# Kernel tuning notes

Measured on AMD Instinct MI355X. Metric: run time of the kernel, lower is better.

## Reference

```python
import jax, jax.numpy as jnp
import numpy as np


def _cheb_conv(x, row, col, norm, W, b, num_nodes):
    # PyG ChebConv with sym normalization and lambda_max=2:
    # L_hat = -D^{-1/2} A D^{-1/2} (off-diagonal), diagonal exactly 0.
    # Tx_0 = x; Tx_1 = L_hat x; Tx_k = 2 L_hat Tx_{k-1} - Tx_{k-2}
    K = W.shape[0]
    Tx0 = x
    out = Tx0 @ W[0]
    Tx1 = jax.ops.segment_sum(norm[:, None] * Tx0[col], row, num_segments=num_nodes)
    out = out + Tx1 @ W[1]
    for k in range(2, K):
        Tx2 = 2.0 * jax.ops.segment_sum(norm[:, None] * Tx1[col], row, num_segments=num_nodes) - Tx0
        out = out + Tx2 @ W[k]
        Tx0, Tx1 = Tx1, Tx2
    return out + b


def setup_inputs() -> dict:
    key = jax.random.key(0)
    ks = jax.random.split(key, 8)
    N, E, D, H, C, K = 100000, 1600000, 128, 64, 5, 3
    x = jax.random.normal(ks[0], (N, D), dtype=jnp.float32)
    edge_index = jax.random.randint(ks[1], (2, E), 0, N, dtype=jnp.int64)
    edge_weight = jax.random.uniform(ks[2], (E,), dtype=jnp.float32)
    s1 = 1.0 / np.sqrt(D)
    s3 = 1.0 / np.sqrt(H)
    W1 = jax.random.normal(ks[3], (K, D, H), dtype=jnp.float32) * s1
    W3 = jax.random.normal(ks[4], (K, H, H), dtype=jnp.float32) * s3
    W4 = jax.random.normal(ks[5], (K, H, C), dtype=jnp.float32) * s3
    return {
        "x": x, "edge_index": edge_index, "edge_weight": edge_weight,
        "W1": W1, "b1": jnp.zeros((H,), jnp.float32),
        "W3": W3, "b3": jnp.zeros((H,), jnp.float32),
        "W4": W4, "b4": jnp.zeros((C,), jnp.float32),
    }


def reference(x, edge_index, edge_weight, W1, b1, W3, b3, W4, b4):
    N = x.shape[0]
    row, col = edge_index[0], edge_index[1]
    # symmetric normalization of the scaled Laplacian (lambda_max = 2)
    deg = jax.ops.segment_sum(edge_weight, row, num_segments=N)
    dinv = jnp.where(deg > 0, jax.lax.rsqrt(jnp.where(deg > 0, deg, 1.0)), 0.0)
    norm = -dinv[row] * edge_weight * dinv[col]
    # dropout is a no-op in eval mode (training=False)
    h = jax.nn.relu(_cheb_conv(x, row, col, norm, W1, b1, N))
    h = jax.nn.relu(_cheb_conv(h, row, col, norm, W3, b3, N))
    h = _cheb_conv(h, row, col, norm, W4, b4, N)
    return jax.nn.log_softmax(h, axis=1)
```

## Files before the change

### kernel.cpp

```cpp
#include <hip/hip_runtime.h>
#include <cstdint>
#include <cstddef>

typedef unsigned short u16;
typedef __attribute__((ext_vector_type(8))) short bf16x8;
typedef __attribute__((ext_vector_type(4))) float f32x4;

#define PB 1024
#define MAXSB 128

__device__ __forceinline__ float bflo(unsigned u) { return __uint_as_float(u << 16); }
__device__ __forceinline__ float bfhi(unsigned u) { return __uint_as_float(u & 0xFFFF0000u); }
__device__ __forceinline__ u16 f2bf(float f) {
    unsigned u = __float_as_uint(f);
    u += 0x7FFFu + ((u >> 16) & 1u);
    return (u16)(u >> 16);
}
__device__ __forceinline__ unsigned pack2(float a, float b) {
    return (unsigned)f2bf(a) | ((unsigned)f2bf(b) << 16);
}


__global__ __launch_bounds__(256) void binA(const int* __restrict__ row, int* __restrict__ P,
                                            int E, int NB, int EB) {
    __shared__ int hist[MAXSB];
    int b = blockIdx.x;
    if (threadIdx.x < MAXSB) hist[threadIdx.x] = 0;
    __syncthreads();
    int e0 = b * EB, e1 = min(E, e0 + EB);
    for (int e = e0 + threadIdx.x; e < e1; e += 256)
        atomicAdd(&hist[row[e] >> 10], 1);
    __syncthreads();
    if (threadIdx.x < NB) P[(size_t)threadIdx.x * PB + b] = hist[threadIdx.x];
}

__global__ __launch_bounds__(256) void binB1(int* __restrict__ P, int* __restrict__ bintot) {
    __shared__ int sh[256];
    int* p = P + (size_t)blockIdx.x * PB;
    int tid = threadIdx.x;
    int base = tid * 4;
    int v[4];
#pragma unroll
    for (int j = 0; j < 4; ++j) v[j] = p[base + j];
    int s = v[0] + v[1] + v[2] + v[3];
    sh[tid] = s;
    __syncthreads();
    for (int off = 1; off < 256; off <<= 1) {
        int t = (tid >= off) ? sh[tid - off] : 0;
        __syncthreads();
        sh[tid] += t;
        __syncthreads();
    }
    int run = sh[tid] - s;
#pragma unroll
    for (int j = 0; j < 4; ++j) { p[base + j] = run; run += v[j]; }
    if (tid == 255) bintot[blockIdx.x] = sh[255];
}

__global__ __launch_bounds__(256) void binC(const int* __restrict__ row, const int* __restrict__ col,
                                            const float* __restrict__ w, const int* __restrict__ P,
                                            const int* __restrict__ bintot, int2* __restrict__ rec,
                                            int E, int NB, int EB) {
    __shared__ int bs[MAXSB];
    __shared__ int cur[MAXSB];
    int b = blockIdx.x;
    int tid = threadIdx.x;
    if (tid < MAXSB) bs[tid] = (tid < NB) ? bintot[tid] : 0;
    __syncthreads();
    for (int off = 1; off < MAXSB; off <<= 1) {
        int t = (tid >= off && tid < MAXSB) ? bs[tid - off] : 0;
        __syncthreads();
        if (tid < MAXSB) bs[tid] += t;
        __syncthreads();
    }
    if (tid < NB) cur[tid] = (tid ? bs[tid - 1] : 0) + P[(size_t)tid * PB + b];
    __syncthreads();
    int e0 = b * EB, e1 = min(E, e0 + EB);
    for (int e = e0 + tid; e < e1; e += 256) {
        int r = row[e];
        int bin = r >> 10;
        int slot = atomicAdd(&cur[bin], 1);
        rec[slot] = make_int2(col[e] | ((r & 1023) << 17), __float_as_int(w[e]));
    }
}

__global__ __launch_bounds__(1024) void binD(const int2* __restrict__ rec,
                                             const int* __restrict__ bintot,
                                             int2* __restrict__ meta, int* __restrict__ rowp,
                                             float* __restrict__ dinv, int N, int NB) {
    __shared__ int bs[MAXSB];
    __shared__ int cnt[1024], st[1024], cur[1024];
    __shared__ float deg[1024];
    int bin = blockIdx.x;
    int tid = threadIdx.x;
    if (tid < MAXSB) bs[tid] = (tid < NB) ? bintot[tid] : 0;
    cnt[tid] = 0;
    deg[tid] = 0.f;
    __syncthreads();
    for (int off = 1; off < MAXSB; off <<= 1) {
        int t = (tid >= off && tid < MAXSB) ? bs[tid - off] : 0;
        __syncthreads();
        if (tid < MAXSB) bs[tid] += t;
        __syncthreads();
    }
    int e0 = bin ? bs[bin - 1] : 0;
    int e1 = bs[bin];
    __syncthreads();
    for (int e = e0 + tid; e < e1; e += 1024) {
        int2 v = rec[e];
        int rl = (v.x >> 17) & 1023;
        atomicAdd(&cnt[rl], 1);
        atomicAdd(&deg[rl], __int_as_float(v.y));
    }
    __syncthreads();
    st[tid] = cnt[tid];
    __syncthreads();
    for (int off = 1; off < 1024; off <<= 1) {
        int t = (tid >= off) ? st[tid - off] : 0;
        __syncthreads();
        st[tid] += t;
        __syncthreads();
    }
    int rows = min(1024, N - bin * 1024);
    int excl = st[tid] - cnt[tid];
    cur[tid] = e0 + excl;
    if (tid < rows) {
        rowp[bin * 1024 + tid] = e0 + excl;
        float d = deg[tid];
        dinv[bin * 1024 + tid] = d > 0.f ? rsqrtf(d) : 0.f;
    }
    if (bin == NB - 1 && tid == 0) rowp[N] = e1;
    __syncthreads();
    for (int e = e0 + tid; e < e1; e += 1024) {
        int2 v = rec[e];
        int rl = (v.x >> 17) & 1023;
        int slot = atomicAdd(&cur[rl], 1);
        meta[slot] = make_int2(v.x & 0x1FFFF, v.y);
    }
}

__global__ void scale_ev(const int* __restrict__ rowp, int2* __restrict__ meta,
                         const float* __restrict__ dinv, int n) {
    int r = blockIdx.x * blockDim.x + threadIdx.x;
    if (r >= n) return;
    int e0 = rowp[r], e1 = rowp[r + 1];
    float dr = dinv[r];
    int e = e0;
    for (; e + 4 <= e1; e += 4) {
        int2 v0 = meta[e], v1 = meta[e + 1], v2 = meta[e + 2], v3 = meta[e + 3];
        float d0 = dinv[v0.x], d1 = dinv[v1.x], d2 = dinv[v2.x], d3 = dinv[v3.x];
        v0.y = __float_as_int(-dr * __int_as_float(v0.y) * d0);
        v1.y = __float_as_int(-dr * __int_as_float(v1.y) * d1);
        v2.y = __float_as_int(-dr * __int_as_float(v2.y) * d2);
        v3.y = __float_as_int(-dr * __int_as_float(v3.y) * d3);
        meta[e] = v0; meta[e + 1] = v1; meta[e + 2] = v2; meta[e + 3] = v3;
    }
    for (; e < e1; ++e) {
        int2 v = meta[e];
        v.y = __float_as_int(-dr * __int_as_float(v.y) * dinv[v.x]);
        meta[e] = v;
    }
}

__global__ void prep(const float* __restrict__ x, unsigned* __restrict__ xb, int n2,
                     const float* __restrict__ W1, const float* __restrict__ W3,
                     const float* __restrict__ W4, u16* __restrict__ Wpu,
                     u16* __restrict__ Wp3, u16* __restrict__ Wpp) {
    int gi = blockIdx.x * blockDim.x + threadIdx.x;
    if (gi < 3072) {
        int idx = gi;
        int lane = idx & 63;
        int nt = (idx >> 6) % 12;
        int kt = idx / 768;
        int krow = kt * 32 + (lane >> 4) * 8;
        int c = nt * 16 + (lane & 15);
        u16 tmp[8];
#pragma unroll
        for (int j = 0; j < 8; ++j) {
            int k = krow + j;
            float v;
            if (c < 64)       v = W1[(size_t)k * 64 + c] - W1[2 * 8192 + (size_t)k * 64 + c];
            else if (c < 128) v = W1[8192 + (size_t)k * 64 + (c - 64)];
            else              v = W1[2 * 8192 + (size_t)k * 64 + (c - 128)];
            tmp[j] = f2bf(v);
        }
        *reinterpret_cast<uint4*>(Wpu + (size_t)idx * 8) = *reinterpret_cast<const uint4*>(tmp);
    } else if (gi < 3072 + 1536) {
        int idx = gi - 3072;
        int lane = idx & 63;
        int nt = (idx >> 6) & 3;
        int kt = idx >> 8;
        int krow = kt * 32 + (lane >> 4) * 8;
        int c = nt * 16 + (lane & 15);
        u16 tmp[8];
#pragma unroll
        for (int j = 0; j < 8; ++j) tmp[j] = f2bf(W3[(size_t)(krow + j) * 64 + c]);
        *reinterpret_cast<uint4*>(Wp3 + (size_t)idx * 8) = *reinterpret_cast<const uint4*>(tmp);
    } else if (gi < 3072 + 1536 + 256) {
        int idx = gi - (3072 + 1536);
        int lane = idx & 63;
        int nt = (idx >> 6) & 1;
        int kt = idx >> 7;
        int krow = kt * 32 + (lane >> 4) * 8;
        int c = nt * 16 + (lane & 15);
        u16 tmp[8];
#pragma unroll
        for (int j = 0; j < 8; ++j) {
            int k = krow + j;
            float v = 0.f;
            if (c < 5)                  v = W4[(size_t)k * 5 + c] - W4[640 + (size_t)k * 5 + c];
            else if (c >= 8 && c < 13)  v = W4[320 + (size_t)k * 5 + (c - 8)];
            else if (c >= 16 && c < 21) v = W4[640 + (size_t)k * 5 + (c - 16)];
            tmp[j] = f2bf(v);
        }
        *reinterpret_cast<uint4*>(Wpp + (size_t)idx * 8) = *reinterpret_cast<const uint4*>(tmp);
    } else {
        int i = gi - 4864;
        if (i < n2) {
            float2 v = reinterpret_cast<const float2*>(x)[i];
            xb[i] = pack2(v.x, v.y);
        }
    }
}

template <int MODE>
__global__ __launch_bounds__(256) void spmm64(const int* __restrict__ rp,
                                              const int2* __restrict__ meta,
                                              const u16* __restrict__ x,
                                              const u16* __restrict__ z,
                                              const float* __restrict__ bias,
                                              u16* __restrict__ y, int n) {
    int r = blockIdx.x * 32 + (threadIdx.x >> 3);
    if (r >= n) return;
    int f = (threadIdx.x & 7) * 8;
    int e0 = rp[r], e1 = rp[r + 1];
    float acc[8] = {0.f, 0.f, 0.f, 0.f, 0.f, 0.f, 0.f, 0.f};
    auto fma8 = [&](uint4 xv, float w) {
        acc[0] += w * bflo(xv.x); acc[1] += w * bfhi(xv.x);
        acc[2] += w * bflo(xv.y); acc[3] += w * bfhi(xv.y);
        acc[4] += w * bflo(xv.z); acc[5] += w * bfhi(xv.z);
        acc[6] += w * bflo(xv.w); acc[7] += w * bfhi(xv.w);
    };
    int e = e0;
    for (; e + 4 <= e1; e += 4) {
        int2 m0 = meta[e], m1 = meta[e + 1], m2 = meta[e + 2], m3 = meta[e + 3];
        uint4 v0 = *reinterpret_cast<const uint4*>(x + (size_t)m0.x * 64 + f);
        uint4 v1 = *reinterpret_cast<const uint4*>(x + (size_t)m1.x * 64 + f);
        uint4 v2 = *reinterpret_cast<const uint4*>(x + (size_t)m2.x * 64 + f);
        uint4 v3 = *reinterpret_cast<const uint4*>(x + (size_t)m3.x * 64 + f);
        fma8(v0, __int_as_float(m0.y));
        fma8(v1, __int_as_float(m1.y));
        fma8(v2, __int_as_float(m2.y));
        fma8(v3, __int_as_float(m3.y));
    }
    for (; e < e1; ++e) {
        int2 m = meta[e];
        uint4 xv = *reinterpret_cast<const uint4*>(x + (size_t)m.x * 64 + f);
        fma8(xv, __int_as_float(m.y));
    }
    if (MODE == 1 || MODE == 2) {
        uint4 zv = *reinterpret_cast<const uint4*>(z + (size_t)r * 64 + f);
        float zz[8] = {bflo(zv.x), bfhi(zv.x), bflo(zv.y), bfhi(zv.y),
                       bflo(zv.z), bfhi(zv.z), bflo(zv.w), bfhi(zv.w)};
#pragma unroll
        for (int j = 0; j < 8; ++j)
            acc[j] = (MODE == 1) ? 2.f * acc[j] + zz[j] : 2.f * acc[j] - zz[j];
    } else if (MODE == 3) {
        uint4 zv = *reinterpret_cast<const uint4*>(z + (size_t)r * 64 + f);
        float zz[8] = {bflo(zv.x), bfhi(zv.x), bflo(zv.y), bfhi(zv.y),
                       bflo(zv.z), bfhi(zv.z), bflo(zv.w), bfhi(zv.w)};
        float4 bl = *reinterpret_cast<const float4*>(bias + f);
        float4 bh = *reinterpret_cast<const float4*>(bias + f + 4);
        float bb[8] = {bl.x, bl.y, bl.z, bl.w, bh.x, bh.y, bh.z, bh.w};
#pragma unroll
        for (int j = 0; j < 8; ++j) acc[j] = fmaxf(acc[j] + zz[j] + bb[j], 0.f);
    }
    uint4 o;
    o.x = pack2(acc[0], acc[1]);
    o.y = pack2(acc[2], acc[3]);
    o.z = pack2(acc[4], acc[5]);
    o.w = pack2(acc[6], acc[7]);
    *reinterpret_cast<uint4*>(y + (size_t)r * 64 + f) = o;
}

__device__ __forceinline__ void spmm8_acc(const int* rp, const int2* meta, const u16* x,
                                          int r, int t, float* acc) {
    int e0 = rp[r], e1 = rp[r + 1];
    auto fma8 = [&](uint4 xv, float w) {
        acc[0] += w * bflo(xv.x); acc[1] += w * bfhi(xv.x);
        acc[2] += w * bflo(xv.y); acc[3] += w * bfhi(xv.y);
        acc[4] += w * bflo(xv.z); acc[5] += w * bfhi(xv.z);
        acc[6] += w * bflo(xv.w); acc[7] += w * bfhi(xv.w);
    };
    int e = e0 + t;
    for (; e + 4 < e1; e += 8) {
        int2 m0 = meta[e], m1 = meta[e + 4];
        uint4 v0 = *reinterpret_cast<const uint4*>(x + (size_t)m0.x * 8);
        uint4 v1 = *reinterpret_cast<const uint4*>(x + (size_t)m1.x * 8);
        fma8(v0, __int_as_float(m0.y));
        fma8(v1, __int_as_float(m1.y));
    }
    for (; e < e1; e += 4) {
        int2 m = meta[e];
        uint4 xv = *reinterpret_cast<const uint4*>(x + (size_t)m.x * 8);
        fma8(xv, __int_as_float(m.y));
    }
#pragma unroll
    for (int j = 0; j < 8; ++j) acc[j] += __shfl_xor(acc[j], 1);
#pragma unroll
    for (int j = 0; j < 8; ++j) acc[j] += __shfl_xor(acc[j], 2);
}

__global__ __launch_bounds__(256) void spmm8_p2(const int* __restrict__ rp,
                                                const int2* __restrict__ meta,
                                                const u16* __restrict__ x,
                                                const u16* __restrict__ z,
                                                u16* __restrict__ y, int n) {
    int r = blockIdx.x * 64 + (threadIdx.x >> 2);
    if (r >= n) return;
    int t = threadIdx.x & 3;
    float acc[8] = {0.f, 0.f, 0.f, 0.f, 0.f, 0.f, 0.f, 0.f};
    spmm8_acc(rp, meta, x, r, t, acc);
    if (t == 0) {
        uint4 zv = *reinterpret_cast<const uint4*>(z + (size_t)r * 8);
        float zz[8] = {bflo(zv.x), bfhi(zv.x), bflo(zv.y), bfhi(zv.y),
                       bflo(zv.z), bfhi(zv.z), bflo(zv.w), bfhi(zv.w)};
        uint4 o;
        o.x = pack2(2.f * acc[0] + zz[0], 2.f * acc[1] + zz[1]);
        o.y = pack2(2.f * acc[2] + zz[2], 2.f * acc[3] + zz[3]);
        o.z = pack2(2.f * acc[4] + zz[4], 2.f * acc[5] + zz[5]);
        o.w = pack2(2.f * acc[6] + zz[6], 2.f * acc[7] + zz[7]);
        *reinterpret_cast<uint4*>(y + (size_t)r * 8) = o;
    }
}

__global__ __launch_bounds__(256) void spmm8_lsm(const int* __restrict__ rp,
                                                 const int2* __restrict__ meta,
                                                 const u16* __restrict__ x,
                                                 const u16* __restrict__ z,
                                                 const float* __restrict__ bias,
                                                 float* __restrict__ out, int n) {
    int r = blockIdx.x * 64 + (threadIdx.x >> 2);
    if (r >= n) return;
    int t = threadIdx.x & 3;
    float acc[8] = {0.f, 0.f, 0.f, 0.f, 0.f, 0.f, 0.f, 0.f};
    spmm8_acc(rp, meta, x, r, t, acc);
    if (t == 0) {
        uint4 zv = *reinterpret_cast<const uint4*>(z + (size_t)r * 8);
        float zz[8] = {bflo(zv.x), bfhi(zv.x), bflo(zv.y), bfhi(zv.y),
                       bflo(zv.z), bfhi(zv.z), bflo(zv.w), bfhi(zv.w)};
        float val[5];
#pragma unroll
        for (int j = 0; j < 5; ++j) val[j] = acc[j] + zz[j] + bias[j];
        float mx = val[0];
#pragma unroll
        for (int j = 1; j < 5; ++j) mx = fmaxf(mx, val[j]);
        float s = 0.f;
#pragma unroll
        for (int j = 0; j < 5; ++j) s += expf(val[j] - mx);
        float l = logf(s);
#pragma unroll
        for (int j = 0; j < 5; ++j) out[(size_t)r * 5 + j] = val[j] - mx - l;
    }
}


__global__ __launch_bounds__(256) void gemm_u(const u16* __restrict__ A,
                                              const u16* __restrict__ Wp,
                                              u16* __restrict__ u0, u16* __restrict__ u1,
                                              u16* __restrict__ u2, int n) {
    int wave = threadIdx.x >> 6;
    int lane = threadIdx.x & 63;
    int r0 = blockIdx.x * 64 + wave * 16;
    int row = r0 + (lane & 15);
    int rowc = row < n ? row : n - 1;
    int kofs = (lane >> 4) * 8;
    f32x4 acc[12] = {};
    for (int kt = 0; kt < 4; ++kt) {
        bf16x8 a = *reinterpret_cast<const bf16x8*>(A + (size_t)rowc * 128 + kt * 32 + kofs);
        const u16* wb = Wp + (size_t)kt * 12 * 512 + (size_t)lane * 8;
#pragma unroll
        for (int nt = 0; nt < 12; ++nt) {
            bf16x8 b = *reinterpret_cast<const bf16x8*>(wb + nt * 512);
            acc[nt] = __builtin_amdgcn_mfma_f32_16x16x32_bf16(a, b, acc[nt], 0, 0, 0);
        }
    }
    int col = lane & 15;
    u16* U[3] = {u0, u1, u2};
#pragma unroll
    for (int nt = 0; nt < 12; ++nt) {
        u16* dst = U[nt >> 2];
        int cc = (nt & 3) * 16 + col;
#pragma unroll
        for (int i = 0; i < 4; ++i) {
            int rr = r0 + (lane >> 4) * 4 + i;
            if (rr < n) dst[(size_t)rr * 64 + cc] = f2bf(acc[nt][i]);
        }
    }
}

__global__ __launch_bounds__(256) void gemm3_mfma(const u16* __restrict__ A0,
                                                  const u16* __restrict__ A1,
                                                  const u16* __restrict__ A2,
                                                  const u16* __restrict__ Wp,
                                                  const float* __restrict__ bias,
                                                  u16* __restrict__ out, int n) {
    int wave = threadIdx.x >> 6;
    int lane = threadIdx.x & 63;
    int r0 = blockIdx.x * 64 + wave * 16;
    int row = r0 + (lane & 15);
    int rowc = row < n ? row : n - 1;
    int kofs = (lane >> 4) * 8;
    const u16* Ap[3] = {A0, A1, A2};
    f32x4 acc[4] = {};
    for (int kt = 0; kt < 6; ++kt) {
        const u16* Asrc = Ap[kt >> 1];
        int c0 = (kt & 1) * 32;
        bf16x8 a = *reinterpret_cast<const bf16x8*>(Asrc + (size_t)rowc * 64 + c0 + kofs);
        const u16* wb = Wp + (size_t)kt * 4 * 512 + (size_t)lane * 8;
#pragma unroll
        for (int nt = 0; nt < 4; ++nt) {
            bf16x8 b = *reinterpret_cast<const bf16x8*>(wb + nt * 512);
            acc[nt] = __builtin_amdgcn_mfma_f32_16x16x32_bf16(a, b, acc[nt], 0, 0, 0);
        }
    }
    int col = lane & 15;
#pragma unroll
    for (int nt = 0; nt < 4; ++nt) {
        float bb = bias[nt * 16 + col];
#pragma unroll
        for (int i = 0; i < 4; ++i) {
            int rr = r0 + (lane >> 4) * 4 + i;
            if (rr < n) {
                float v = fmaxf(acc[nt][i] + bb, 0.f);
                out[(size_t)rr * 64 + nt * 16 + col] = f2bf(v);
            }
        }
    }
}

__global__ __launch_bounds__(256) void gemm_proj(const u16* __restrict__ A,
                                                 const u16* __restrict__ Wp,
                                                 u16* __restrict__ p0, u16* __restrict__ p1,
                                                 u16* __restrict__ p2, int n) {
    int wave = threadIdx.x >> 6;
    int lane = threadIdx.x & 63;
    int r0 = blockIdx.x * 64 + wave * 16;
    int row = r0 + (lane & 15);
    int rowc = row < n ? row : n - 1;
    int kofs = (lane >> 4) * 8;
    f32x4 acc[2] = {};
    for (int kt = 0; kt < 2; ++kt) {
        bf16x8 a = *reinterpret_cast<const bf16x8*>(A + (size_t)rowc * 64 + kt * 32 + kofs);
        const u16* wb = Wp + (size_t)kt * 2 * 512 + (size_t)lane * 8;
#pragma unroll
        for (int nt = 0; nt < 2; ++nt) {
            bf16x8 b = *reinterpret_cast<const bf16x8*>(wb + nt * 512);
            acc[nt] = __builtin_amdgcn_mfma_f32_16x16x32_bf16(a, b, acc[nt], 0, 0, 0);
        }
    }
    int col = lane & 15;
    u16* P[3] = {p0, p1, p2};
#pragma unroll
    for (int nt = 0; nt < 2; ++nt) {
        int c = nt * 16 + col;
        if (c < 24) {
            u16* dst = P[c >> 3];
            int j = c & 7;
#pragma unroll
            for (int i = 0; i < 4; ++i) {
                int rr = r0 + (lane >> 4) * 4 + i;
                if (rr < n) dst[(size_t)rr * 8 + j] = f2bf(acc[nt][i]);
            }
        }
    }
}


static inline size_t alignup(size_t v) { return (v + 255) & ~(size_t)255; }

extern "C" void kernel_launch(void* const* d_in, const int* in_sizes, int n_in,
                              void* d_out, int out_size, void* d_ws, size_t ws_size,
                              hipStream_t stream) {
    const float* x  = (const float*)d_in[0];
    const int*   ei = (const int*)d_in[1];
    const float* ew = (const float*)d_in[2];
    const float* W1 = (const float*)d_in[3];
    const float* b1 = (const float*)d_in[4];
    const float* W3 = (const float*)d_in[5];
    const float* b3 = (const float*)d_in[6];
    const float* W4 = (const float*)d_in[7];
    const float* b4 = (const float*)d_in[8];
    float* out = (float*)d_out;

    const int D = 128, H = 64;
    const int N = in_sizes[0] / D;
    const int E = in_sizes[2];
    const int* row = ei;
    const int* col = ei + E;

    char* ws = (char*)d_ws;
    size_t off = 0;
    auto alloc = [&](size_t bytes) { size_t o = off; off += alignup(bytes); return o; };

    float* dinv   = (float*)(ws + alloc((size_t)N * 4));
    int*   rowp   = (int*)  (ws + alloc((size_t)(N + 1) * 4));
    int*   bintot = (int*)  (ws + alloc(MAXSB * 4));
    int*   P      = (int*)  (ws + alloc((size_t)MAXSB * PB * 4));
    int2*  meta   = (int2*) (ws + alloc((size_t)E * 8));
    int2*  rec    = (int2*) (ws + alloc((size_t)E * 8));
    u16*   xb     = (u16*)  (ws + alloc((size_t)N * D * 2));
    u16*   A      = (u16*)  (ws + alloc((size_t)N * H * 2));
    u16*   B      = (u16*)  (ws + alloc((size_t)N * H * 2));
    u16*   C      = (u16*)  (ws + alloc((size_t)N * H * 2));
    u16*   Dd     = (u16*)  (ws + alloc((size_t)N * H * 2));
    u16*   P0     = (u16*)  (ws + alloc((size_t)N * 8 * 2));
    u16*   P1     = (u16*)  (ws + alloc((size_t)N * 8 * 2));
    u16*   P2     = (u16*)  (ws + alloc((size_t)N * 8 * 2));
    u16*   P3     = (u16*)  (ws + alloc((size_t)N * 8 * 2));
    u16*   Wpu    = (u16*)  (ws + alloc((size_t)4 * 12 * 512 * 2));
    u16*   Wp3    = (u16*)  (ws + alloc((size_t)6 * 4 * 512 * 2));
    u16*   Wpp    = (u16*)  (ws + alloc((size_t)2 * 2 * 512 * 2));

    const int NB = (N + 1023) >> 10;
    const int EB = (E + PB - 1) / PB;

    dim3 blk(256);
    int gN = (N + 255) / 256;

    binA<<<PB, blk, 0, stream>>>(row, P, E, NB, EB);
    binB1<<<NB, blk, 0, stream>>>(P, bintot);
    binC<<<PB, blk, 0, stream>>>(row, col, ew, P, bintot, rec, E, NB, EB);
    binD<<<NB, dim3(1024), 0, stream>>>(rec, bintot, meta, rowp, dinv, N, NB);
    scale_ev<<<gN, blk, 0, stream>>>(rowp, meta, dinv, N);

    int n2 = N * D / 2;
    prep<<<(n2 + 4864 + 255) / 256, blk, 0, stream>>>(x, (unsigned*)xb, n2, W1, W3, W4,
                                                      Wpu, Wp3, Wpp);

    int g64 = (N + 31) / 32;
    int gG  = (N + 63) / 64;
    int g8  = (N + 63) / 64;

    gemm_u<<<gG, blk, 0, stream>>>(xb, Wpu, A, B, C, N);
    spmm64<1><<<g64, blk, 0, stream>>>(rowp, meta, C, B, nullptr, Dd, N);
    spmm64<3><<<g64, blk, 0, stream>>>(rowp, meta, Dd, A, b1, B, N);

    spmm64<0><<<g64, blk, 0, stream>>>(rowp, meta, B, nullptr, nullptr, C, N);
    spmm64<2><<<g64, blk, 0, stream>>>(rowp, meta, C, B, nullptr, A, N);
    gemm3_mfma<<<gG, blk, 0, stream>>>(B, C, A, Wp3, b3, Dd, N);

    gemm_proj<<<gG, blk, 0, stream>>>(Dd, Wpp, P0, P1, P2, N);
    spmm8_p2<<<g8, blk, 0, stream>>>(rowp, meta, P2, P1, P3, N);
    spmm8_lsm<<<g8, blk, 0, stream>>>(rowp, meta, P3, P0, b4, out, N);
}
```

Before: 308.5 us.

## Split CSR build into degree and scatter passes, fuse normalization into scatter

Coarse bins shrink from 1024 to 512 rows, so there are about twice as many 256-thread blocks. The old single binD kernel is split into binD1, which computes counts, degrees, row pointers and dinv with a wave-shuffle scan, and binD2, which places edges in CSR order. binD2 computes the normalized edge weight during placement, so the separate scale_ev pass over meta is removed. It records a local permutation in shared memory so that meta writes are contiguous, at the cost of a second read of rec and a 48KB shared array that may limit occupancy.

```diff
diff --git a/kernel.cpp b/kernel.cpp
--- a/kernel.cpp
+++ b/kernel.cpp
@@ -7,7 +7,9 @@
 typedef __attribute__((ext_vector_type(4))) float f32x4;
 
 #define PB 1024
-#define MAXSB 128
+#define MAXSB 256
+#define SB 512
+#define CAP 12288
 
 __device__ __forceinline__ float bflo(unsigned u) { return __uint_as_float(u << 16); }
 __device__ __forceinline__ float bfhi(unsigned u) { return __uint_as_float(u & 0xFFFF0000u); }
@@ -25,11 +27,11 @@
                                             int E, int NB, int EB) {
     __shared__ int hist[MAXSB];
     int b = blockIdx.x;
-    if (threadIdx.x < MAXSB) hist[threadIdx.x] = 0;
+    hist[threadIdx.x] = 0;
     __syncthreads();
     int e0 = b * EB, e1 = min(E, e0 + EB);
     for (int e = e0 + threadIdx.x; e < e1; e += 256)
-        atomicAdd(&hist[row[e] >> 10], 1);
+        atomicAdd(&hist[row[e] >> 9], 1);
     __syncthreads();
     if (threadIdx.x < NB) P[(size_t)threadIdx.x * PB + b] = hist[threadIdx.x];
 }
@@ -55,6 +57,17 @@
 #pragma unroll
     for (int j = 0; j < 4; ++j) { p[base + j] = run; run += v[j]; }
     if (tid == 255) bintot[blockIdx.x] = sh[255];
+}
+
+__device__ __forceinline__ void bs_scan(int* bs, const int* bintot, int NB, int tid) {
+    bs[tid] = (tid < NB) ? bintot[tid] : 0;
+    __syncthreads();
+    for (int off = 1; off < 256; off <<= 1) {
+        int t = (tid >= off) ? bs[tid - off] : 0;
+        __syncthreads();
+        bs[tid] += t;
+        __syncthreads();
+    }
 }
 
 __global__ __launch_bounds__(256) void binC(const int* __restrict__ row, const int* __restrict__ col,
@@ -65,100 +78,111 @@
     __shared__ int cur[MAXSB];
     int b = blockIdx.x;
     int tid = threadIdx.x;
-    if (tid < MAXSB) bs[tid] = (tid < NB) ? bintot[tid] : 0;
-    __syncthreads();
-    for (int off = 1; off < MAXSB; off <<= 1) {
-        int t = (tid >= off && tid < MAXSB) ? bs[tid - off] : 0;
-        __syncthreads();
-        if (tid < MAXSB) bs[tid] += t;
-        __syncthreads();
-    }
+    bs_scan(bs, bintot, NB, tid);
     if (tid < NB) cur[tid] = (tid ? bs[tid - 1] : 0) + P[(size_t)tid * PB + b];
     __syncthreads();
     int e0 = b * EB, e1 = min(E, e0 + EB);
     for (int e = e0 + tid; e < e1; e += 256) {
         int r = row[e];
-        int bin = r >> 10;
+        int bin = r >> 9;
         int slot = atomicAdd(&cur[bin], 1);
-        rec[slot] = make_int2(col[e] | ((r & 1023) << 17), __float_as_int(w[e]));
-    }
-}
-
-__global__ __launch_bounds__(1024) void binD(const int2* __restrict__ rec,
+        rec[slot] = make_int2(col[e] | ((r & 511) << 17), __float_as_int(w[e]));
+    }
+}
+
+__global__ __launch_bounds__(256) void binD1(const int2* __restrict__ rec,
                                              const int* __restrict__ bintot,
-                                             int2* __restrict__ meta, int* __restrict__ rowp,
-                                             float* __restrict__ dinv, int N, int NB) {
+                                             int* __restrict__ rowp, float* __restrict__ dinv,
+                                             int N, int NB) {
     __shared__ int bs[MAXSB];
-    __shared__ int cnt[1024], st[1024], cur[1024];
-    __shared__ float deg[1024];
+    __shared__ int cnt[SB];
+    __shared__ float deg[SB];
+    __shared__ int wsum[4];
     int bin = blockIdx.x;
     int tid = threadIdx.x;
-    if (tid < MAXSB) bs[tid] = (tid < NB) ? bintot[tid] : 0;
-    cnt[tid] = 0;
-    deg[tid] = 0.f;
-    __syncthreads();
-    for (int off = 1; off < MAXSB; off <<= 1) {
-        int t = (tid >= off && tid < MAXSB) ? bs[tid - off] : 0;
-        __syncthreads();
-        if (tid < MAXSB) bs[tid] += t;
-        __syncthreads();
-    }
+    bs_scan(bs, bintot, NB, tid);
     int e0 = bin ? bs[bin - 1] : 0;
     int e1 = bs[bin];
-    __syncthreads();
-    for (int e = e0 + tid; e < e1; e += 1024) {
+    cnt[tid] = 0; cnt[tid + 256] = 0;
+    deg[tid] = 0.f; deg[tid + 256] = 0.f;
+    __syncthreads();
+    for (int e = e0 + tid; e < e1; e += 256) {
         int2 v = rec[e];
-        int rl = (v.x >> 17) & 1023;
+        int rl = (v.x >> 17) & 511;
         atomicAdd(&cnt[rl], 1);
         atomicAdd(&deg[rl], __int_as_float(v.y));
     }
     __syncthreads();
-    st[tid] = cnt[tid];
-    __syncthreads();
-    for (int off = 1; off < 1024; off <<= 1) {
-        int t = (tid >= off) ? st[tid - off] : 0;
-        __syncthreads();
-        st[tid] += t;
-        __syncthreads();
-    }
-    int rows = min(1024, N - bin * 1024);
-    int excl = st[tid] - cnt[tid];
-    cur[tid] = e0 + excl;
-    if (tid < rows) {
-        rowp[bin * 1024 + tid] = e0 + excl;
-        float d = deg[tid];
-        dinv[bin * 1024 + tid] = d > 0.f ? rsqrtf(d) : 0.f;
+    int a = cnt[2 * tid], b = cnt[2 * tid + 1];
+    int p = a + b;
+    int lane = tid & 63, wv = tid >> 6;
+    int incl = p;
+    for (int off = 1; off < 64; off <<= 1) {
+        int t = __shfl_up(incl, off);
+        if (lane >= off) incl += t;
+    }
+    if (lane == 63) wsum[wv] = incl;
+    __syncthreads();
+    if (tid == 0) {
+        int s = 0;
+#pragma unroll
+        for (int i = 0; i < 4; ++i) { int t = wsum[i]; wsum[i] = s; s += t; }
+    }
+    __syncthreads();
+    int excl = incl - p + wsum[wv];
+    int base = bin * SB;
+    int rows = min(SB, N - base);
+    if (2 * tid < rows) {
+        rowp[base + 2 * tid] = e0 + excl;
+        float d = deg[2 * tid];
+        dinv[base + 2 * tid] = d > 0.f ? rsqrtf(d) : 0.f;
+    }
+    if (2 * tid + 1 < rows) {
+        rowp[base + 2 * tid + 1] = e0 + excl + a;
+        float d = deg[2 * tid + 1];
+        dinv[base + 2 * tid + 1] = d > 0.f ? rsqrtf(d) : 0.f;
     }
     if (bin == NB - 1 && tid == 0) rowp[N] = e1;
-    __syncthreads();
-    for (int e = e0 + tid; e < e1; e += 1024) {
+}
+
+__global__ __launch_bounds__(256) void binD2(const int2* __restrict__ rec,
+                                             const int* __restrict__ bintot,
+                                             const int* __restrict__ rowp,
+                                             const float* __restrict__ dinv,
+                                             int2* __restrict__ meta, int N, int NB) {
+    __shared__ int bs[MAXSB];
+    __shared__ int cur[SB];
+    __shared__ int perm[CAP];
+    int bin = blockIdx.x;
+    int tid = threadIdx.x;
+    bs_scan(bs, bintot, NB, tid);
+    int e0 = bin ? bs[bin - 1] : 0;
+    int e1 = bs[bin];
+    int base = bin * SB;
+    int rows = min(SB, N - base);
+    for (int i = tid; i < rows; i += 256) cur[i] = rowp[base + i];
+    __syncthreads();
+    for (int e = e0 + tid; e < e1; e += 256) {
         int2 v = rec[e];
-        int rl = (v.x >> 17) & 1023;
+        int rl = (v.x >> 17) & 511;
         int slot = atomicAdd(&cur[rl], 1);
-        meta[slot] = make_int2(v.x & 0x1FFFF, v.y);
-    }
-}
-
-__global__ void scale_ev(const int* __restrict__ rowp, int2* __restrict__ meta,
-                         const float* __restrict__ dinv, int n) {
-    int r = blockIdx.x * blockDim.x + threadIdx.x;
-    if (r >= n) return;
-    int e0 = rowp[r], e1 = rowp[r + 1];
-    float dr = dinv[r];
-    int e = e0;
-    for (; e + 4 <= e1; e += 4) {
-        int2 v0 = meta[e], v1 = meta[e + 1], v2 = meta[e + 2], v3 = meta[e + 3];
-        float d0 = dinv[v0.x], d1 = dinv[v1.x], d2 = dinv[v2.x], d3 = dinv[v3.x];
-        v0.y = __float_as_int(-dr * __int_as_float(v0.y) * d0);
-        v1.y = __float_as_int(-dr * __int_as_float(v1.y) * d1);
-        v2.y = __float_as_int(-dr * __int_as_float(v2.y) * d2);
-        v3.y = __float_as_int(-dr * __int_as_float(v3.y) * d3);
-        meta[e] = v0; meta[e + 1] = v1; meta[e + 2] = v2; meta[e + 3] = v3;
-    }
-    for (; e < e1; ++e) {
-        int2 v = meta[e];
-        v.y = __float_as_int(-dr * __int_as_float(v.y) * dinv[v.x]);
-        meta[e] = v;
+        int so = slot - e0;
+        if (so < CAP) {
+            perm[so] = e - e0;
+        } else {
+            int c = v.x & 0x1FFFF;
+            float ev = -dinv[base + rl] * __int_as_float(v.y) * dinv[c];
+            meta[slot] = make_int2(c, __float_as_int(ev));
+        }
+    }
+    __syncthreads();
+    int lim = min(e1 - e0, CAP);
+    for (int s = tid; s < lim; s += 256) {
+        int2 v = rec[e0 + perm[s]];
+        int rl = (v.x >> 17) & 511;
+        int c = v.x & 0x1FFFF;
+        float ev = -dinv[base + rl] * __int_as_float(v.y) * dinv[c];
+        meta[e0 + s] = make_int2(c, __float_as_int(ev));
     }
 }
 
@@ -522,17 +546,16 @@
     u16*   Wp3    = (u16*)  (ws + alloc((size_t)6 * 4 * 512 * 2));
     u16*   Wpp    = (u16*)  (ws + alloc((size_t)2 * 2 * 512 * 2));
 
-    const int NB = (N + 1023) >> 10;
+    const int NB = (N + SB - 1) / SB;
     const int EB = (E + PB - 1) / PB;
 
     dim3 blk(256);
-    int gN = (N + 255) / 256;
 
     binA<<<PB, blk, 0, stream>>>(row, P, E, NB, EB);
     binB1<<<NB, blk, 0, stream>>>(P, bintot);
     binC<<<PB, blk, 0, stream>>>(row, col, ew, P, bintot, rec, E, NB, EB);
-    binD<<<NB, dim3(1024), 0, stream>>>(rec, bintot, meta, rowp, dinv, N, NB);
-    scale_ev<<<gN, blk, 0, stream>>>(rowp, meta, dinv, N);
+    binD1<<<NB, blk, 0, stream>>>(rec, bintot, rowp, dinv, N, NB);
+    binD2<<<NB, blk, 0, stream>>>(rec, bintot, rowp, dinv, meta, N, NB);
 
     int n2 = N * D / 2;
     prep<<<(n2 + 4864 + 255) / 256, blk, 0, stream>>>(x, (unsigned*)xb, n2, W1, W3, W4,
```

Result: faster. 284.7 us (-7.7%).
